# Kernel tuning notes

Measured on AMD Instinct MI355X. Metric: run time of the kernel, lower is better.

Reference implementation:

```python
import jax, jax.numpy as jnp
import numpy as np

HIDDEN = 1024
HEADS = 16
HEAD_DIM = HIDDEN // HEADS

def setup_inputs() -> dict:
    key = jax.random.key(0)
    k1, k2, k3 = jax.random.split(key, 3)
    scale = 1.0 / np.sqrt(HIDDEN)
    return {
        "x": jax.random.normal(k1, (2, 2048, HIDDEN), dtype=jnp.float32),
        "w_qkv": jax.random.normal(k2, (HIDDEN, 3 * HIDDEN), dtype=jnp.float32) * scale,
        "b_qkv": jnp.zeros((3 * HIDDEN,), dtype=jnp.float32),
        "w_out": jax.random.normal(k3, (HIDDEN, HIDDEN), dtype=jnp.float32) * scale,
        "b_out": jnp.zeros((HIDDEN,), dtype=jnp.float32),
    }

def reference(x, w_qkv, b_qkv, w_out, b_out):
    B, S, H = x.shape
    qkv = x @ w_qkv + b_qkv                              # (B,S,3H)
    qkv = qkv.reshape(B, S, 3, HEADS, HEAD_DIM)
    qkv = jnp.transpose(qkv, (2, 0, 3, 1, 4))            # (3,B,nh,S,hd)
    q, k, v = qkv[0], qkv[1], qkv[2]
    scores = jnp.einsum("bhqd,bhkd->bhqk", q, k) / np.sqrt(HEAD_DIM)
    causal = jnp.triu(jnp.ones((S, S), dtype=bool), k=1)  # True above diagonal
    scores = jnp.where(causal, -jnp.inf, scores)
    attn = jax.nn.softmax(scores, axis=-1)               # dropout: eval mode (identity)
    out = jnp.einsum("bhqk,bhkd->bhqd", attn, v)
    out = jnp.transpose(out, (0, 2, 1, 3)).reshape(B, S, H)
    return out @ w_out + b_out
```

## Files before the change

kernel.cpp:

```cpp
#include <hip/hip_runtime.h>
#include <hip/hip_bf16.h>

typedef short short8 __attribute__((ext_vector_type(8)));
typedef float f32x4 __attribute__((ext_vector_type(4)));

typedef const __attribute__((address_space(1))) unsigned int* gas_ptr;
typedef __attribute__((address_space(3))) unsigned int* las_ptr;
#define ASYNC16(g, l) __builtin_amdgcn_global_load_lds((gas_ptr)(g), (las_ptr)(l), 16, 0, 0)

__device__ __forceinline__ unsigned short f2bf(float f) {
    unsigned int u = __builtin_bit_cast(unsigned int, f);
    u += 0x7fff + ((u >> 16) & 1);
    return (unsigned short)(u >> 16);
}
__device__ __forceinline__ float bf2f(unsigned short s) {
    unsigned int u = (unsigned int)s << 16;
    return __builtin_bit_cast(float, u);
}
__device__ __forceinline__ unsigned int pkbf_trunc(float lo, float hi) {
    return __builtin_amdgcn_perm(__builtin_bit_cast(unsigned int, hi),
                                 __builtin_bit_cast(unsigned int, lo), 0x07060302u);
}
__device__ __forceinline__ float fexp2(float x) {
#if __has_builtin(__builtin_amdgcn_exp2f)
    return __builtin_amdgcn_exp2f(x);
#else
    return __expf(x * 0.6931471805599453f);
#endif
}

__device__ __forceinline__ void transpose_tile(
    const float* __restrict__ w, unsigned short* __restrict__ wt,
    int K, int N, int k0, int n0, unsigned short* tile)
{
    for (int i = threadIdx.x; i < 64 * 64; i += 256) {
        int r = i >> 6, c = i & 63;
        tile[r * 65 + c] = f2bf(w[(size_t)(k0 + r) * N + n0 + c]);
    }
    __syncthreads();
    for (int i = threadIdx.x; i < 64 * 64; i += 256) {
        int r = i >> 6, c = i & 63;
        wt[(size_t)(n0 + r) * K + k0 + c] = tile[c * 65 + r];
    }
}

__global__ __launch_bounds__(256) void prep(
    const float* __restrict__ x, const float* __restrict__ w_qkv,
    const float* __restrict__ w_out,
    unsigned short* __restrict__ x_b, unsigned short* __restrict__ wqkv_t,
    unsigned short* __restrict__ wout_t)
{
    __shared__ unsigned short tile[64 * 65];
    int bid = blockIdx.x;
    if (bid < 4096) {
        int i = (bid * 256 + threadIdx.x) * 4;
        float4 v = *(const float4*)(x + i);
        ushort4 o;
        o.x = f2bf(v.x); o.y = f2bf(v.y); o.z = f2bf(v.z); o.w = f2bf(v.w);
        *(ushort4*)(x_b + i) = o;
    } else if (bid < 4096 + 768) {
        int t = bid - 4096;
        transpose_tile(w_qkv, wqkv_t, 1024, 3072, (t / 48) * 64, (t % 48) * 64, tile);
    } else {
        int t = bid - 4864;
        transpose_tile(w_out, wout_t, 1024, 1024, (t >> 4) * 64, (t & 15) * 64, tile);
    }
}


template<bool OUT_BF16, bool QKV>
__global__ __launch_bounds__(256, 3) void gemm_bt(
    const unsigned short* __restrict__ A,
    const unsigned short* __restrict__ Bt,
    const float* __restrict__ bias,
    void* __restrict__ C,
    unsigned short* __restrict__ vTp,
    int M, int N, int K)
{
    __shared__ __align__(16) unsigned short As[128 * 32];
    __shared__ __align__(16) unsigned short Bs[128 * 32];
    const int tid = threadIdx.x;
    const int lane = tid & 63;
    const int wave = tid >> 6;
    const int wr = wave >> 1, wc = wave & 1;
    const int m0 = blockIdx.x * 128, n0 = blockIdx.y * 128;
    const int fr = lane & 15, fq = lane >> 4;

    f32x4 acc[4][4] = {};

    const int grow = lane >> 2;
    const int gcol = (lane & 3) * 8;
    const unsigned short* Ag = A  + (size_t)(m0 + wave * 32 + grow) * K + gcol;
    const unsigned short* Bg = Bt + (size_t)(n0 + wave * 32 + grow) * K + gcol;
    unsigned short* AsW0 = As + (wave * 32) * 32;
    unsigned short* AsW1 = As + (wave * 32 + 16) * 32;
    unsigned short* BsW0 = Bs + (wave * 32) * 32;
    unsigned short* BsW1 = Bs + (wave * 32 + 16) * 32;

    for (int k0 = 0; k0 < K; k0 += 32) {
        __syncthreads();
        ASYNC16(Ag + k0,          AsW0);
        ASYNC16(Ag + 16 * K + k0, AsW1);
        ASYNC16(Bg + k0,          BsW0);
        ASYNC16(Bg + 16 * K + k0, BsW1);
        __syncthreads();

        short8 af[4], bfr[4];
#pragma unroll
        for (int i = 0; i < 4; i++)
            af[i] = *(const short8*)(As + (wr * 64 + i * 16 + fr) * 32 + fq * 8);
#pragma unroll
        for (int j = 0; j < 4; j++)
            bfr[j] = *(const short8*)(Bs + (wc * 64 + j * 16 + fr) * 32 + fq * 8);
#pragma unroll
        for (int i = 0; i < 4; i++)
#pragma unroll
            for (int j = 0; j < 4; j++)
                acc[i][j] = __builtin_amdgcn_mfma_f32_16x16x32_bf16(af[i], bfr[j], acc[i][j], 0, 0, 0);
    }

#pragma unroll
    for (int i = 0; i < 4; i++)
#pragma unroll
        for (int j = 0; j < 4; j++) {
            int col = n0 + wc * 64 + j * 16 + fr;
            float bv = bias[col];
            if (QKV && col >= 2048) {
                int hh = (col - 2048) >> 6, d = col & 63;
#pragma unroll
                for (int r = 0; r < 4; r++) {
                    int row = m0 + wr * 64 + i * 16 + fq * 4 + r;
                    int bb = row >> 11, s = row & 2047;
                    vTp[((size_t)(bb * 16 + hh) * 64 + d) * 2048 + s] = f2bf(acc[i][j][r] + bv);
                }
            } else {
                const int cstride = QKV ? 2048 : N;
#pragma unroll
                for (int r = 0; r < 4; r++) {
                    int row = m0 + wr * 64 + i * 16 + fq * 4 + r;
                    float v = acc[i][j][r] + bv;
                    if (OUT_BF16)
                        ((unsigned short*)C)[(size_t)row * cstride + col] = f2bf(v);
                    else
                        ((float*)C)[(size_t)row * cstride + col] = v;
                }
            }
        }
}


template<int RG0>
__device__ __forceinline__ void attn_step(
    const unsigned short* __restrict__ Ks0, const unsigned short* __restrict__ Ks1,
    const unsigned short* __restrict__ Vs0, const unsigned short* __restrict__ Vs1,
    unsigned short* __restrict__ Psw,
    const short8 (&qf)[4][2], const short8 ones,
    f32x4 (&o_acc)[4][4], f32x4 (&l_acc)[4],
    int j0, int fr, int fq,
    const int (&qrow0)[4], bool diagA, bool diagB)
{
    const int kpos = ((fq + (fr >> 1)) & 3) * 8;
    short8 kf[4][2];
#pragma unroll
    for (int t = 0; t < 4; t++) {
        kf[t][0] = *(const short8*)(Ks0 + (t * 16 + fr) * 32 + kpos);
        kf[t][1] = *(const short8*)(Ks1 + (t * 16 + fr) * 32 + kpos);
    }

    const float C1 = 0.18033688011112042f;
    const float C2 = -11.541560327111707f;

#pragma unroll
    for (int rg = RG0; rg < 4; rg++) {
        f32x4 s[4];
        __builtin_amdgcn_s_setprio(1);
#pragma unroll
        for (int t = 0; t < 4; t++) {
            s[t] = (f32x4){0.f, 0.f, 0.f, 0.f};
            s[t] = __builtin_amdgcn_mfma_f32_16x16x32_bf16(kf[t][0], qf[rg][0], s[t], 0, 0, 0);
            s[t] = __builtin_amdgcn_mfma_f32_16x16x32_bf16(kf[t][1], qf[rg][1], s[t], 0, 0, 0);
        }
        __builtin_amdgcn_s_setprio(0);
        const bool diag = (rg < 2) ? diagA : diagB;
        unsigned short* prow = Psw + rg * (16 * 64);
        const int qr = qrow0[rg] + fr;
        if (diag) {
#pragma unroll
            for (int t = 0; t < 4; t++) {
                const int kb = j0 + t * 16 + fq * 4;
                float p[4];
#pragma unroll
                for (int r = 0; r < 4; r++) {
                    float v = fexp2(s[t][r] * C1 + C2);
                    if (kb + r > qr) v = 0.f;
                    p[r] = v;
                }
                uint2 pk;
                pk.x = pkbf_trunc(p[0], p[1]);
                pk.y = pkbf_trunc(p[2], p[3]);
                const int blk = (t * 2 + (fq >> 1) + fr) & 7;
                *(uint2*)(prow + fr * 64 + blk * 8 + (fq & 1) * 4) = pk;
            }
        } else {
#pragma unroll
            for (int t = 0; t < 4; t++) {
                float p[4];
#pragma unroll
                for (int r = 0; r < 4; r++)
                    p[r] = fexp2(s[t][r] * C1 + C2);
                uint2 pk;
                pk.x = pkbf_trunc(p[0], p[1]);
                pk.y = pkbf_trunc(p[2], p[3]);
                const int blk = (t * 2 + (fq >> 1) + fr) & 7;
                *(uint2*)(prow + fr * 64 + blk * 8 + (fq & 1) * 4) = pk;
            }
        }
    }

#pragma unroll
    for (int ks = 0; ks < 2; ks++) {
        const unsigned short* Vsb = ks ? Vs1 : Vs0;
        const int colp = ((ks * 4 + fq + fr) & 7) * 8;
        short8 pf[4];
#pragma unroll
        for (int rg = RG0; rg < 4; rg++)
            pf[rg] = *(const short8*)(Psw + rg * (16 * 64) + fr * 64 + colp);
        __builtin_amdgcn_s_setprio(1);
#pragma unroll
        for (int t = 0; t < 4; t++) {
            short8 vf = *(const short8*)(Vsb + (t * 16 + fr) * 32 + kpos);
#pragma unroll
            for (int rg = RG0; rg < 4; rg++)
                o_acc[rg][t] = __builtin_amdgcn_mfma_f32_16x16x32_bf16(pf[rg], vf, o_acc[rg][t], 0, 0, 0);
        }
#pragma unroll
        for (int rg = RG0; rg < 4; rg++)
            l_acc[rg] = __builtin_amdgcn_mfma_f32_16x16x32_bf16(pf[rg], ones, l_acc[rg], 0, 0, 0);
        __builtin_amdgcn_s_setprio(0);
    }
}

__global__ __launch_bounds__(128, 2) void flash_attn(
    const unsigned short* __restrict__ qkv,
    const unsigned short* __restrict__ vT,
    unsigned short* __restrict__ Opart,
    float* __restrict__ lpart)
{
    const int p = blockIdx.x;
    const int g = blockIdx.y;
    const int h = blockIdx.z & 15, b = blockIdx.z >> 4;
    const int tid = threadIdx.x, wave = tid >> 6, lane = tid & 63;
    const int fr = lane & 15, fq = lane >> 4;
    const size_t RS = 2048;

    const unsigned short* Qb = qkv + (size_t)b * 2048 * RS + h * 64;
    const unsigned short* Kb = Qb + 1024;
    const unsigned short* Vt = vT + (size_t)(b * 16 + h) * 64 * 2048;

    __shared__ __align__(16) unsigned short Ks[2][64 * 32];
    __shared__ __align__(16) unsigned short Vs[2][64 * 32];
    __shared__ __align__(16) unsigned short Ps[2][4 * 16 * 64];

    short8 qf[4][2];
    int qrow0[4];
#pragma unroll
    for (int rg = 0; rg < 4; rg++) {
        int qt = (rg < 2) ? p : (31 - p);
        qrow0[rg] = qt * 64 + wave * 32 + (rg & 1) * 16;
        const unsigned short* qrow = Qb + (size_t)(qrow0[rg] + fr) * RS;
        qf[rg][0] = *(const short8*)(qrow + fq * 8);
        qf[rg][1] = *(const short8*)(qrow + 32 + fq * 8);
    }
    short8 ones;
#pragma unroll
    for (int e = 0; e < 8; e++) ones[e] = (short)0x3F80;

    f32x4 o_acc[4][4] = {};
    f32x4 l_acc[4] = {};

    const int grow = lane >> 2;
    const int gcol = (((lane & 3) - (grow >> 1)) & 3) * 8;
    const unsigned short* Kg = Kb + (size_t)(wave * 32 + grow) * RS + gcol;
    const unsigned short* Vg = Vt + (size_t)(wave * 32 + grow) * 2048 + gcol;
    unsigned short* KsW00 = Ks[0] + (wave * 32) * 32;
    unsigned short* KsW01 = Ks[0] + (wave * 32 + 16) * 32;
    unsigned short* KsW10 = Ks[1] + (wave * 32) * 32;
    unsigned short* KsW11 = Ks[1] + (wave * 32 + 16) * 32;
    unsigned short* VsW00 = Vs[0] + (wave * 32) * 32;
    unsigned short* VsW01 = Vs[0] + (wave * 32 + 16) * 32;
    unsigned short* VsW10 = Vs[1] + (wave * 32) * 32;
    unsigned short* VsW11 = Vs[1] + (wave * 32 + 16) * 32;

    const int c8 = 8 * (p + 1);
    const int T0 = g * 33, T1 = T0 + 33;
    const int lo = (T0 <= c8) ? ((T0 + 4) >> 3) : (p + 1 + ((T0 - c8 + 2) >> 2));
    const int hi = (T1 <= c8) ? ((T1 + 4) >> 3) : (p + 1 + ((T1 - c8 + 2) >> 2));

    for (int jt = lo; jt < hi; jt++) {
        const int j0 = jt * 64;
        __syncthreads();
        ASYNC16(Kg + (size_t)j0 * RS,               KsW00);
        ASYNC16(Kg + (size_t)(j0 + 16) * RS,        KsW01);
        ASYNC16(Kg + (size_t)j0 * RS + 32,          KsW10);
        ASYNC16(Kg + (size_t)(j0 + 16) * RS + 32,   KsW11);
        ASYNC16(Vg + j0,                  VsW00);
        ASYNC16(Vg + 16 * 2048 + j0,      VsW01);
        ASYNC16(Vg + j0 + 32,             VsW10);
        ASYNC16(Vg + 16 * 2048 + j0 + 32, VsW11);
        __syncthreads();

        bool diagA = (jt == p), diagB = (jt == 31 - p);
        if (jt <= p)
            attn_step<0>(Ks[0], Ks[1], Vs[0], Vs[1], Ps[wave], qf, ones,
                         o_acc, l_acc, j0, fr, fq, qrow0, diagA, diagB);
        else
            attn_step<2>(Ks[0], Ks[1], Vs[0], Vs[1], Ps[wave], qf, ones,
                         o_acc, l_acc, j0, fr, fq, qrow0, diagA, diagB);
    }

    unsigned short* Og = Opart + (size_t)g * 4096 * 1024;
    float* lg = lpart + (size_t)g * 4096 * 16;
#pragma unroll
    for (int rg = 0; rg < 4; rg++) {
#pragma unroll
        for (int t = 0; t < 4; t++)
#pragma unroll
            for (int r = 0; r < 4; r++) {
                int row = qrow0[rg] + fq * 4 + r;
                Og[(size_t)(b * 2048 + row) * 1024 + h * 64 + t * 16 + fr] = f2bf(o_acc[rg][t][r]);
            }
        if (fr == 0) {
#pragma unroll
            for (int r = 0; r < 4; r++) {
                int row = qrow0[rg] + fq * 4 + r;
                lg[(size_t)(b * 2048 + row) * 16 + h] = l_acc[rg][r];
            }
        }
    }
}

__global__ __launch_bounds__(256) void reduce_attn(
    const unsigned short* __restrict__ Opart, const float* __restrict__ lpart,
    unsigned short* __restrict__ out)
{
    int i = (blockIdx.x * 256 + threadIdx.x) * 8;
    int row = i >> 10, h = (i & 1023) >> 6;
    float lsum = 0.f;
#pragma unroll
    for (int g = 0; g < 4; g++)
        lsum += lpart[(size_t)g * 4096 * 16 + row * 16 + h];
    float inv = 1.0f / lsum;
    float acc[8] = {0.f, 0.f, 0.f, 0.f, 0.f, 0.f, 0.f, 0.f};
#pragma unroll
    for (int g = 0; g < 4; g++) {
        const unsigned short* Op = Opart + (size_t)g * 4096 * 1024 + i;
        ushort4 a0 = *(const ushort4*)(Op);
        ushort4 a1 = *(const ushort4*)(Op + 4);
        acc[0] += bf2f(a0.x); acc[1] += bf2f(a0.y); acc[2] += bf2f(a0.z); acc[3] += bf2f(a0.w);
        acc[4] += bf2f(a1.x); acc[5] += bf2f(a1.y); acc[6] += bf2f(a1.z); acc[7] += bf2f(a1.w);
    }
    ushort4 o0, o1;
    o0.x = f2bf(acc[0] * inv); o0.y = f2bf(acc[1] * inv);
    o0.z = f2bf(acc[2] * inv); o0.w = f2bf(acc[3] * inv);
    o1.x = f2bf(acc[4] * inv); o1.y = f2bf(acc[5] * inv);
    o1.z = f2bf(acc[6] * inv); o1.w = f2bf(acc[7] * inv);
    *(ushort4*)(out + i) = o0;
    *(ushort4*)(out + i + 4) = o1;
}

extern "C" void kernel_launch(void* const* d_in, const int* in_sizes, int n_in,
                              void* d_out, int out_size, void* d_ws, size_t ws_size,
                              hipStream_t stream) {
    const float* x      = (const float*)d_in[0];
    const float* w_qkv  = (const float*)d_in[1];
    const float* b_qkv  = (const float*)d_in[2];
    const float* w_out  = (const float*)d_in[3];
    const float* b_out  = (const float*)d_in[4];
    float* out = (float*)d_out;

    char* ws = (char*)d_ws;
    unsigned short* x_b    = (unsigned short*)(ws);
    unsigned short* wqkv_t = (unsigned short*)(ws + 8u  * 1024 * 1024);
    unsigned short* wout_t = (unsigned short*)(ws + 14u * 1024 * 1024);
    unsigned short* qkv    = (unsigned short*)(ws + 16u * 1024 * 1024);
    unsigned short* attn   = (unsigned short*)(ws + 32u * 1024 * 1024);
    unsigned short* vT     = (unsigned short*)(ws + 40u * 1024 * 1024);
    unsigned short* Opart  = (unsigned short*)(ws + 48u * 1024 * 1024);
    float*          lpart  = (float*)         (ws + 80u * 1024 * 1024);

    prep<<<5120, 256, 0, stream>>>(x, w_qkv, w_out, x_b, wqkv_t, wout_t);
    gemm_bt<true, true ><<<dim3(32, 24), 256, 0, stream>>>(x_b,  wqkv_t, b_qkv, qkv, vT, 4096, 3072, 1024);
    flash_attn<<<dim3(16, 4, 32), 128, 0, stream>>>(qkv, vT, Opart, lpart);
    reduce_attn<<<2048, 256, 0, stream>>>(Opart, lpart, attn);
    gemm_bt<false, false><<<dim3(32, 8),  256, 0, stream>>>(attn, wout_t, b_out, out, nullptr, 4096, 1024, 1024);
}
```

Before: 196.9 us.

## Load K/V fragments directly from global and split attention work into two partitions

The flash attention kernel no longer stages K and V tiles through LDS with async copies and barriers. Each wave now reads its MFMA fragments straight from global memory, relying on L1/L2 for reuse between the two waves. The key range is split into two partitions per query-tile pair instead of four, so the grid halves and the reduce kernel sums two partials. This removes the barriers and LDS traffic but duplicates global loads across waves, loses latency hiding from async prefetch, and lowers parallelism.

Measured after the change: 230.4 us. +17.0%, slower.

```diff
diff --git a/kernel.cpp b/kernel.cpp
--- a/kernel.cpp
+++ b/kernel.cpp
@@ -151,20 +151,27 @@
 
 template<int RG0>
 __device__ __forceinline__ void attn_step(
-    const unsigned short* __restrict__ Ks0, const unsigned short* __restrict__ Ks1,
-    const unsigned short* __restrict__ Vs0, const unsigned short* __restrict__ Vs1,
+    const unsigned short* __restrict__ Kj,
+    const unsigned short* __restrict__ Vj,
     unsigned short* __restrict__ Psw,
     const short8 (&qf)[4][2], const short8 ones,
     f32x4 (&o_acc)[4][4], f32x4 (&l_acc)[4],
     int j0, int fr, int fq,
     const int (&qrow0)[4], bool diagA, bool diagB)
 {
-    const int kpos = ((fq + (fr >> 1)) & 3) * 8;
     short8 kf[4][2];
 #pragma unroll
     for (int t = 0; t < 4; t++) {
-        kf[t][0] = *(const short8*)(Ks0 + (t * 16 + fr) * 32 + kpos);
-        kf[t][1] = *(const short8*)(Ks1 + (t * 16 + fr) * 32 + kpos);
+        const unsigned short* kr = Kj + (size_t)(t * 16 + fr) * 2048 + fq * 8;
+        kf[t][0] = *(const short8*)(kr);
+        kf[t][1] = *(const short8*)(kr + 32);
+    }
+    short8 vf0[4], vf1[4];
+#pragma unroll
+    for (int t = 0; t < 4; t++) {
+        const unsigned short* vr = Vj + (size_t)(t * 16 + fr) * 2048 + fq * 8;
+        vf0[t] = *(const short8*)(vr);
+        vf1[t] = *(const short8*)(vr + 32);
     }
 
     const float C1 = 0.18033688011112042f;
@@ -219,7 +226,6 @@
 
 #pragma unroll
     for (int ks = 0; ks < 2; ks++) {
-        const unsigned short* Vsb = ks ? Vs1 : Vs0;
         const int colp = ((ks * 4 + fq + fr) & 7) * 8;
         short8 pf[4];
 #pragma unroll
@@ -228,10 +234,10 @@
         __builtin_amdgcn_s_setprio(1);
 #pragma unroll
         for (int t = 0; t < 4; t++) {
-            short8 vf = *(const short8*)(Vsb + (t * 16 + fr) * 32 + kpos);
+            short8 vv = ks ? vf1[t] : vf0[t];
 #pragma unroll
             for (int rg = RG0; rg < 4; rg++)
-                o_acc[rg][t] = __builtin_amdgcn_mfma_f32_16x16x32_bf16(pf[rg], vf, o_acc[rg][t], 0, 0, 0);
+                o_acc[rg][t] = __builtin_amdgcn_mfma_f32_16x16x32_bf16(pf[rg], vv, o_acc[rg][t], 0, 0, 0);
         }
 #pragma unroll
         for (int rg = RG0; rg < 4; rg++)
@@ -257,8 +263,6 @@
     const unsigned short* Kb = Qb + 1024;
     const unsigned short* Vt = vT + (size_t)(b * 16 + h) * 64 * 2048;
 
-    __shared__ __align__(16) unsigned short Ks[2][64 * 32];
-    __shared__ __align__(16) unsigned short Vs[2][64 * 32];
     __shared__ __align__(16) unsigned short Ps[2][4 * 16 * 64];
 
     short8 qf[4][2];
@@ -278,43 +282,18 @@
     f32x4 o_acc[4][4] = {};
     f32x4 l_acc[4] = {};
 
-    const int grow = lane >> 2;
-    const int gcol = (((lane & 3) - (grow >> 1)) & 3) * 8;
-    const unsigned short* Kg = Kb + (size_t)(wave * 32 + grow) * RS + gcol;
-    const unsigned short* Vg = Vt + (size_t)(wave * 32 + grow) * 2048 + gcol;
-    unsigned short* KsW00 = Ks[0] + (wave * 32) * 32;
-    unsigned short* KsW01 = Ks[0] + (wave * 32 + 16) * 32;
-    unsigned short* KsW10 = Ks[1] + (wave * 32) * 32;
-    unsigned short* KsW11 = Ks[1] + (wave * 32 + 16) * 32;
-    unsigned short* VsW00 = Vs[0] + (wave * 32) * 32;
-    unsigned short* VsW01 = Vs[0] + (wave * 32 + 16) * 32;
-    unsigned short* VsW10 = Vs[1] + (wave * 32) * 32;
-    unsigned short* VsW11 = Vs[1] + (wave * 32 + 16) * 32;
-
-    const int c8 = 8 * (p + 1);
-    const int T0 = g * 33, T1 = T0 + 33;
-    const int lo = (T0 <= c8) ? ((T0 + 4) >> 3) : (p + 1 + ((T0 - c8 + 2) >> 2));
-    const int hi = (T1 <= c8) ? ((T1 + 4) >> 3) : (p + 1 + ((T1 - c8 + 2) >> 2));
+    const int mid = (p >= 8) ? 8 : (16 - p);
+    const int lo = g ? mid : 0;
+    const int hi = g ? (32 - p) : mid;
 
     for (int jt = lo; jt < hi; jt++) {
         const int j0 = jt * 64;
-        __syncthreads();
-        ASYNC16(Kg + (size_t)j0 * RS,               KsW00);
-        ASYNC16(Kg + (size_t)(j0 + 16) * RS,        KsW01);
-        ASYNC16(Kg + (size_t)j0 * RS + 32,          KsW10);
-        ASYNC16(Kg + (size_t)(j0 + 16) * RS + 32,   KsW11);
-        ASYNC16(Vg + j0,                  VsW00);
-        ASYNC16(Vg + 16 * 2048 + j0,      VsW01);
-        ASYNC16(Vg + j0 + 32,             VsW10);
-        ASYNC16(Vg + 16 * 2048 + j0 + 32, VsW11);
-        __syncthreads();
-
         bool diagA = (jt == p), diagB = (jt == 31 - p);
         if (jt <= p)
-            attn_step<0>(Ks[0], Ks[1], Vs[0], Vs[1], Ps[wave], qf, ones,
+            attn_step<0>(Kb + (size_t)j0 * RS, Vt + j0, Ps[wave], qf, ones,
                          o_acc, l_acc, j0, fr, fq, qrow0, diagA, diagB);
         else
-            attn_step<2>(Ks[0], Ks[1], Vs[0], Vs[1], Ps[wave], qf, ones,
+            attn_step<2>(Kb + (size_t)j0 * RS, Vt + j0, Ps[wave], qf, ones,
                          o_acc, l_acc, j0, fr, fq, qrow0, diagA, diagB);
     }
 
@@ -345,25 +324,21 @@
 {
     int i = (blockIdx.x * 256 + threadIdx.x) * 8;
     int row = i >> 10, h = (i & 1023) >> 6;
-    float lsum = 0.f;
-#pragma unroll
-    for (int g = 0; g < 4; g++)
-        lsum += lpart[(size_t)g * 4096 * 16 + row * 16 + h];
+    float lsum = lpart[(size_t)row * 16 + h] + lpart[(size_t)4096 * 16 + row * 16 + h];
     float inv = 1.0f / lsum;
-    float acc[8] = {0.f, 0.f, 0.f, 0.f, 0.f, 0.f, 0.f, 0.f};
-#pragma unroll
-    for (int g = 0; g < 4; g++) {
-        const unsigned short* Op = Opart + (size_t)g * 4096 * 1024 + i;
-        ushort4 a0 = *(const ushort4*)(Op);
-        ushort4 a1 = *(const ushort4*)(Op + 4);
-        acc[0] += bf2f(a0.x); acc[1] += bf2f(a0.y); acc[2] += bf2f(a0.z); acc[3] += bf2f(a0.w);
-        acc[4] += bf2f(a1.x); acc[5] += bf2f(a1.y); acc[6] += bf2f(a1.z); acc[7] += bf2f(a1.w);
-    }
+    ushort4 a0 = *(const ushort4*)(Opart + i);
+    ushort4 a1 = *(const ushort4*)(Opart + i + 4);
+    ushort4 b0 = *(const ushort4*)(Opart + (size_t)4096 * 1024 + i);
+    ushort4 b1 = *(const ushort4*)(Opart + (size_t)4096 * 1024 + i + 4);
     ushort4 o0, o1;
-    o0.x = f2bf(acc[0] * inv); o0.y = f2bf(acc[1] * inv);
-    o0.z = f2bf(acc[2] * inv); o0.w = f2bf(acc[3] * inv);
-    o1.x = f2bf(acc[4] * inv); o1.y = f2bf(acc[5] * inv);
-    o1.z = f2bf(acc[6] * inv); o1.w = f2bf(acc[7] * inv);
+    o0.x = f2bf((bf2f(a0.x) + bf2f(b0.x)) * inv);
+    o0.y = f2bf((bf2f(a0.y) + bf2f(b0.y)) * inv);
+    o0.z = f2bf((bf2f(a0.z) + bf2f(b0.z)) * inv);
+    o0.w = f2bf((bf2f(a0.w) + bf2f(b0.w)) * inv);
+    o1.x = f2bf((bf2f(a1.x) + bf2f(b1.x)) * inv);
+    o1.y = f2bf((bf2f(a1.y) + bf2f(b1.y)) * inv);
+    o1.z = f2bf((bf2f(a1.z) + bf2f(b1.z)) * inv);
+    o1.w = f2bf((bf2f(a1.w) + bf2f(b1.w)) * inv);
     *(ushort4*)(out + i) = o0;
     *(ushort4*)(out + i + 4) = o1;
 }
@@ -386,11 +361,11 @@
     unsigned short* attn   = (unsigned short*)(ws + 32u * 1024 * 1024);
     unsigned short* vT     = (unsigned short*)(ws + 40u * 1024 * 1024);
     unsigned short* Opart  = (unsigned short*)(ws + 48u * 1024 * 1024);
-    float*          lpart  = (float*)         (ws + 80u * 1024 * 1024);
+    float*          lpart  = (float*)         (ws + 64u * 1024 * 1024);
 
     prep<<<5120, 256, 0, stream>>>(x, w_qkv, w_out, x_b, wqkv_t, wout_t);
     gemm_bt<true, true ><<<dim3(32, 24), 256, 0, stream>>>(x_b,  wqkv_t, b_qkv, qkv, vT, 4096, 3072, 1024);
-    flash_attn<<<dim3(16, 4, 32), 128, 0, stream>>>(qkv, vT, Opart, lpart);
+    flash_attn<<<dim3(16, 2, 32), 128, 0, stream>>>(qkv, vT, Opart, lpart);
     reduce_attn<<<2048, 256, 0, stream>>>(Opart, lpart, attn);
     gemm_bt<false, false><<<dim3(32, 8),  256, 0, stream>>>(attn, wout_t, b_out, out, nullptr, 4096, 1024, 1024);
 }
```
